# Performance work log

Hardware: AMD Instinct MI355X
Metric: run time of the kernel (lower is better)

## Reference

```python
import jax, jax.numpy as jnp
import numpy as np
from jax import lax

CHUNK = 256  # query chunk size (manual tiling block)

def setup_inputs() -> dict:
    key = jax.random.key(0)
    kq, kk, kv = jax.random.split(key, 3)
    shape = (2, 16, 2048, 128)  # [B, H, S, D]
    q = jax.random.normal(kq, shape, dtype=jnp.float32)
    k = jax.random.normal(kk, shape, dtype=jnp.float32)
    v = jax.random.normal(kv, shape, dtype=jnp.float32)
    return {"q": q, "k": k, "v": v}

def reference(q, k, v):
    # Chunked (memory-efficient) exact attention: softmax(QK^T/sqrt(D)) V,
    # computed one query block at a time so the full [S,S] score matrix
    # is never materialized.
    B, H, S, D = q.shape
    scale = jnp.asarray(1.0 / np.sqrt(D), dtype=q.dtype)
    n_chunks = S // CHUNK
    # [n_chunks, B, H, CHUNK, D]
    q_blocks = q.reshape(B, H, n_chunks, CHUNK, D).transpose(2, 0, 1, 3, 4)

    def step(carry, q_blk):
        # scores for this query block vs all keys: [B, H, CHUNK, S]
        s = jnp.einsum('bhqd,bhkd->bhqk', q_blk, k) * scale
        p = jax.nn.softmax(s, axis=-1)
        o = jnp.einsum('bhqk,bhkd->bhqd', p, v)
        return carry, o

    _, out_blocks = lax.scan(step, None, q_blocks)
    # [n_chunks, B, H, CHUNK, D] -> [B, H, S, D]
    out = out_blocks.transpose(1, 2, 0, 3, 4).reshape(B, H, S, D)
    return out
```

## Files before the change

### kernel.cpp

```cpp
#include <hip/hip_runtime.h>
#include <hip/hip_bf16.h>


typedef short short8 __attribute__((ext_vector_type(8)));
typedef float f32x16 __attribute__((ext_vector_type(16)));

#define MFMA32(a, b, c) __builtin_amdgcn_mfma_f32_32x32x16_bf16((a), (b), (c), 0, 0, 0)

#if __has_builtin(__builtin_amdgcn_exp2f)
#define EXP2(x) __builtin_amdgcn_exp2f(x)
#else
#define EXP2(x) exp2f(x)
#endif

constexpr int Dh  = 128;
constexpr int S_  = 2048;
constexpr int KVB = 64;
constexpr int NT  = S_ / KVB;
constexpr int WAVES = 8;
constexpr int QBLK  = 256;

__device__ __forceinline__ short f2bf(float f) {
    union { float f; unsigned u; } x; x.f = f;
    unsigned r = x.u + 0x7fffu + ((x.u >> 16) & 1u);
    return (short)(r >> 16);
}

__device__ __forceinline__ unsigned pkbf(float lo, float hi) {
    unsigned r;
    asm("v_cvt_pk_bf16_f32 %0, %1, %2" : "=v"(r) : "v"(lo), "v"(hi));
    return r;
}

__device__ __forceinline__ void pswap(unsigned &a, unsigned &b) {
    asm("v_permlane32_swap_b32 %0, %1" : "+v"(a), "+v"(b));
}

__device__ __forceinline__ void gload16(const void* g, void* l) {
    __builtin_amdgcn_global_load_lds(
        (const __attribute__((address_space(1))) unsigned int*)g,
        (__attribute__((address_space(3))) unsigned int*)l, 16, 0, 0);
}

__global__ __launch_bounds__(256) void prep_k(const float* __restrict__ K,
                                              short* __restrict__ Kz) {
    int idx = blockIdx.x * 256 + threadIdx.x;
    int b   = idx & 15;
    int s   = (idx >> 4) & (S_ - 1);
    int sb  = b ^ (s & 15);
    const float* src = K + (size_t)(idx >> 4) * Dh + sb * 8;
    float4 f0 = ((const float4*)src)[0];
    float4 f1 = ((const float4*)src)[1];
    short8 o;
    o[0] = f2bf(f0.x); o[1] = f2bf(f0.y); o[2] = f2bf(f0.z); o[3] = f2bf(f0.w);
    o[4] = f2bf(f1.x); o[5] = f2bf(f1.y); o[6] = f2bf(f1.z); o[7] = f2bf(f1.w);
    *(short8*)(Kz + (size_t)idx * 8) = o;
}

__global__ __launch_bounds__(256) void prep_v(const float* __restrict__ V,
                                              short* __restrict__ Vt) {
    __shared__ short tr[64][72];
    int bid = blockIdx.x;
    int dg = bid & 1, seg = (bid >> 1) & 31, bh = bid >> 6;
    int t = threadIdx.x;
    int s = t >> 2, d0 = (t & 3) * 16;
    const float* src = V + (size_t)(bh * S_ + seg * 64 + s) * Dh + dg * 64 + d0;
    #pragma unroll
    for (int i = 0; i < 16; i += 4) {
        float4 f = *(const float4*)(src + i);
        tr[d0 + i + 0][s] = f2bf(f.x); tr[d0 + i + 1][s] = f2bf(f.y);
        tr[d0 + i + 2][s] = f2bf(f.z); tr[d0 + i + 3][s] = f2bf(f.w);
    }
    __syncthreads();
    int d = t >> 2, j0 = (t & 3) * 2;
    size_t ob = ((size_t)(bh * 32 + seg) * 128 + dg * 64 + d) * 64;
    #pragma unroll
    for (int jj = 0; jj < 2; ++jj) {
        int j = j0 + jj;
        int sj = (j ^ (d & 7)) * 8;
        short8 val = *(const short8*)&tr[d][sj];
        *(short8*)(Vt + ob + j * 8) = val;
    }
}

__global__ __launch_bounds__(512, 2)
void mea_fwd6(const float* __restrict__ Qg, const short* __restrict__ Kz,
              const short* __restrict__ Vt, float* __restrict__ Og, int nqt) {
    __shared__ __align__(16) short kbuf[3][KVB * Dh];
    __shared__ __align__(16) short vbuf[3][Dh * KVB];
    __shared__ float bc_lds[WAVES][32];

    const int bid = blockIdx.x;
    const int cpx = (int)gridDim.x >> 3;
    const int swz = (bid & 7) * cpx + (bid >> 3);
    const int qt  = swz % nqt;
    const int bh  = swz / nqt;

    const int tid  = threadIdx.x;
    const int w    = tid >> 6;
    const int lane = tid & 63;
    const int l31  = lane & 31;
    const int hi   = lane >> 5;

    const size_t base = (size_t)bh * S_ * Dh;
    const int    qrow = qt * QBLK + w * 32 + l31;
    const float  QSC  = 0.08838834764831845f * 1.4426950408889634f;

    short8 qf[8];
    {
        const float* qp = Qg + base + (size_t)qrow * Dh;
        #pragma unroll
        for (int kc = 0; kc < 8; ++kc) {
            const float4 f0 = *(const float4*)(qp + kc * 16 + hi * 8);
            const float4 f1 = *(const float4*)(qp + kc * 16 + hi * 8 + 4);
            short8 a;
            a[0] = f2bf(f0.x * QSC); a[1] = f2bf(f0.y * QSC);
            a[2] = f2bf(f0.z * QSC); a[3] = f2bf(f0.w * QSC);
            a[4] = f2bf(f1.x * QSC); a[5] = f2bf(f1.y * QSC);
            a[6] = f2bf(f1.z * QSC); a[7] = f2bf(f1.w * QSC);
            qf[kc] = a;
        }
    }

    f32x16 oacc[4];
    #pragma unroll
    for (int dt = 0; dt < 4; ++dt)
        #pragma unroll
        for (int r = 0; r < 16; ++r) oacc[dt][r] = 0.f;
    float mrun = -1e30f, lpart = 0.f;

    const short* kt0 = Kz + base;
    const short* vt0 = Vt + base;

    short *kA = kbuf[0], *kB = kbuf[1], *kC = kbuf[2];
    short *vA = vbuf[0], *vB = vbuf[1], *vC = vbuf[2];

    auto STAGE = [&](short* kl, short* vl, int t) {
        const short* ks = kt0 + (size_t)t * (KVB * Dh);
        const short* vs = vt0 + (size_t)t * (Dh * KVB);
        #pragma unroll
        for (int i = 0; i < 2; ++i) {
            const int ou = (i * 8 + w) * 512;
            gload16(ks + ou + lane * 8, kl + ou);
            gload16(vs + ou + lane * 8, vl + ou);
        }
    };

    auto QKSTEP = [&](const short* kl, f32x16& A, f32x16& B) {
        #pragma unroll
        for (int r = 0; r < 16; ++r) { A[r] = 0.f; B[r] = 0.f; }
        __builtin_amdgcn_s_setprio(1);
        #pragma unroll
        for (int kc = 0; kc < 8; ++kc) {
            const int go = (((kc * 2 + hi) ^ (l31 & 15)) * 8);
            const short8 a0 = *(const short8*)&kl[l31 * Dh + go];
            const short8 a1 = *(const short8*)&kl[(32 + l31) * Dh + go];
            A = MFMA32(a0, qf[kc], A);
            B = MFMA32(a1, qf[kc], B);
        }
        __builtin_amdgcn_s_setprio(0);
    };

    auto SMPACK = [&](f32x16& sa, f32x16& sb, short8* pf) {
        float mxl = sa[0];
        #pragma unroll
        for (int r = 1; r < 16; ++r) mxl = fmaxf(mxl, sa[r]);
        #pragma unroll
        for (int r = 0; r < 16; ++r) mxl = fmaxf(mxl, sb[r]);
        if (__any(mxl > mrun + 8.0f)) {
            float mo   = fmaxf(mxl, __shfl_xor(mxl, 32));
            float mnew = fmaxf(mrun, mo);
            float rc   = EXP2(mrun - mnew);
            mrun = mnew;
            lpart *= rc;
            if (!hi) bc_lds[w][l31] = rc;
            #pragma unroll
            for (int m = 0; m < 4; ++m) {
                const float4 rcv = *(const float4*)&bc_lds[w][m * 8 + 4 * hi];
                #pragma unroll
                for (int t2 = 0; t2 < 4; ++t2) {
                    const float f = (&rcv.x)[t2];
                    #pragma unroll
                    for (int dt = 0; dt < 4; ++dt) oacc[dt][m * 4 + t2] *= f;
                }
            }
        }
        f32x16 pa, pb;
        float s0 = 0.f, s1 = 0.f;
        #pragma unroll
        for (int r = 0; r < 16; ++r) { pa[r] = EXP2(sa[r] - mrun); s0 += pa[r]; }
        #pragma unroll
        for (int r = 0; r < 16; ++r) { pb[r] = EXP2(sb[r] - mrun); s1 += pb[r]; }
        lpart += s0 + s1;
        #pragma unroll
        for (int kk = 0; kk < 2; ++kk) {
            unsigned a0 = pkbf(pa[kk * 8 + 0], pa[kk * 8 + 1]);
            unsigned a1 = pkbf(pa[kk * 8 + 2], pa[kk * 8 + 3]);
            unsigned b0 = pkbf(pa[kk * 8 + 4], pa[kk * 8 + 5]);
            unsigned b1 = pkbf(pa[kk * 8 + 6], pa[kk * 8 + 7]);
            pswap(a0, b0); pswap(a1, b1);
            unsigned wd[4] = {a0, a1, b0, b1};
            pf[kk] = *(const short8*)wd;
        }
        #pragma unroll
        for (int kk = 0; kk < 2; ++kk) {
            unsigned a0 = pkbf(pb[kk * 8 + 0], pb[kk * 8 + 1]);
            unsigned a1 = pkbf(pb[kk * 8 + 2], pb[kk * 8 + 3]);
            unsigned b0 = pkbf(pb[kk * 8 + 4], pb[kk * 8 + 5]);
            unsigned b1 = pkbf(pb[kk * 8 + 6], pb[kk * 8 + 7]);
            pswap(a0, b0); pswap(a1, b1);
            unsigned wd[4] = {a0, a1, b0, b1};
            pf[2 + kk] = *(const short8*)wd;
        }
    };

    auto PVSTEP = [&](const short* vl, const short8* pf) {
        __builtin_amdgcn_s_setprio(1);
        #pragma unroll
        for (int dt = 0; dt < 4; ++dt) {
            #pragma unroll
            for (int ks = 0; ks < 4; ++ks) {
                const short8 bv = *(const short8*)
                    &vl[(dt * 32 + l31) * KVB + (((ks * 2 + hi) ^ (l31 & 7)) * 8)];
                oacc[dt] = MFMA32(pf[ks], bv, oacc[dt]);
            }
        }
        __builtin_amdgcn_s_setprio(0);
    };

    auto BODY = [&](int t, f32x16& cA, f32x16& cB, f32x16& nA, f32x16& nB) {
        if (t + 2 < NT) STAGE(kC, vC, t + 2);
        QKSTEP(kB, nA, nB);
        short8 pf[4];
        SMPACK(cA, cB, pf);
        PVSTEP(vA, pf);
        __syncthreads();
        short* tk = kA; kA = kB; kB = kC; kC = tk;
        short* tv = vA; vA = vB; vB = vC; vC = tv;
    };

    STAGE(kA, vA, 0);
    STAGE(kB, vB, 1);
    __syncthreads();
    f32x16 s0A, s0B, s1A, s1B;
    QKSTEP(kA, s0A, s0B);

    #pragma unroll 1
    for (int kk = 0; kk < 15; ++kk) {
        BODY(2 * kk,     s0A, s0B, s1A, s1B);
        BODY(2 * kk + 1, s1A, s1B, s0A, s0B);
    }
    BODY(30, s0A, s0B, s1A, s1B);
    {
        short8 pf[4];
        SMPACK(s1A, s1B, pf);
        PVSTEP(vA, pf);
    }

    {
        const float tot = lpart + __shfl_xor(lpart, 32);
        if (!hi) bc_lds[w][l31] = 1.0f / tot;
    }
    float* op = Og + base;
    #pragma unroll
    for (int m = 0; m < 4; ++m) {
        const float4 li = *(const float4*)&bc_lds[w][m * 8 + 4 * hi];
        #pragma unroll
        for (int t2 = 0; t2 < 4; ++t2) {
            const int row  = m * 8 + 4 * hi + t2;
            const float lf = (&li.x)[t2];
            #pragma unroll
            for (int dt = 0; dt < 4; ++dt)
                op[(size_t)(qt * QBLK + w * 32 + row) * Dh + dt * 32 + l31]
                    = oacc[dt][m * 4 + t2] * lf;
        }
    }
}

typedef float f32x4 __attribute__((ext_vector_type(4)));
#define MFMA16(a, b, c) __builtin_amdgcn_mfma_f32_16x16x32_bf16((a), (b), (c), 0, 0, 0)
constexpr int FKVB = 32;
constexpr int FKP  = 136;
constexpr int FVP  = 40;
constexpr int FPP  = 40;

__global__ __launch_bounds__(256, 2)
void mea_fwd_fb(const float* __restrict__ Qg, const float* __restrict__ Kg,
                const float* __restrict__ Vg, float* __restrict__ Og,
                int S, int nqt) {
    __shared__ __align__(16) short k_lds[FKVB][FKP];
    __shared__ __align__(16) short vT_lds[Dh][FVP];
    __shared__ __align__(16) short p_lds[4][16][FPP];

    const int qt = blockIdx.x % nqt;
    const int bh = blockIdx.x / nqt;
    const int tid = threadIdx.x;
    const int w = tid >> 6, lane = tid & 63;
    const int lr = lane & 15, lg = lane >> 4;
    const size_t base = (size_t)bh * S * Dh;
    const int qrow0 = qt * 64 + w * 16;
    const float scale = 0.08838834764831845f;

    short8 qf[4];
    {
        const float* qp = Qg + base + (size_t)(qrow0 + lr) * Dh;
        #pragma unroll
        for (int kc = 0; kc < 4; ++kc) {
            const float4 f0 = *(const float4*)(qp + kc * 32 + lg * 8);
            const float4 f1 = *(const float4*)(qp + kc * 32 + lg * 8 + 4);
            short8 a;
            a[0] = f2bf(f0.x); a[1] = f2bf(f0.y); a[2] = f2bf(f0.z); a[3] = f2bf(f0.w);
            a[4] = f2bf(f1.x); a[5] = f2bf(f1.y); a[6] = f2bf(f1.z); a[7] = f2bf(f1.w);
            qf[kc] = a;
        }
    }
    f32x4 oacc[8];
    #pragma unroll
    for (int dt = 0; dt < 8; ++dt) oacc[dt] = (f32x4){0.f, 0.f, 0.f, 0.f};
    float mrun[4] = {-1e30f, -1e30f, -1e30f, -1e30f};
    float lrun[4] = {0.f, 0.f, 0.f, 0.f};
    const int sr = tid >> 3, sc = (tid & 7) * 16;

    for (int kv0 = 0; kv0 < S; kv0 += FKVB) {
        {
            const float* kp = Kg + base + (size_t)(kv0 + sr) * Dh + sc;
            const float* vp = Vg + base + (size_t)(kv0 + sr) * Dh + sc;
            short8 pk0, pk1;
            float4 f0 = ((const float4*)kp)[0], f1 = ((const float4*)kp)[1];
            float4 f2 = ((const float4*)kp)[2], f3 = ((const float4*)kp)[3];
            pk0[0] = f2bf(f0.x); pk0[1] = f2bf(f0.y); pk0[2] = f2bf(f0.z); pk0[3] = f2bf(f0.w);
            pk0[4] = f2bf(f1.x); pk0[5] = f2bf(f1.y); pk0[6] = f2bf(f1.z); pk0[7] = f2bf(f1.w);
            pk1[0] = f2bf(f2.x); pk1[1] = f2bf(f2.y); pk1[2] = f2bf(f2.z); pk1[3] = f2bf(f2.w);
            pk1[4] = f2bf(f3.x); pk1[5] = f2bf(f3.y); pk1[6] = f2bf(f3.z); pk1[7] = f2bf(f3.w);
            *(short8*)&k_lds[sr][sc] = pk0;
            *(short8*)&k_lds[sr][sc + 8] = pk1;
            #pragma unroll
            for (int i = 0; i < 4; ++i) {
                float4 f = ((const float4*)vp)[i];
                vT_lds[sc + 4 * i + 0][sr] = f2bf(f.x);
                vT_lds[sc + 4 * i + 1][sr] = f2bf(f.y);
                vT_lds[sc + 4 * i + 2][sr] = f2bf(f.z);
                vT_lds[sc + 4 * i + 3][sr] = f2bf(f.w);
            }
        }
        __syncthreads();
        f32x4 s0 = (f32x4){0.f,0.f,0.f,0.f}, s1 = (f32x4){0.f,0.f,0.f,0.f};
        #pragma unroll
        for (int kc = 0; kc < 4; ++kc) {
            short8 b0 = *(const short8*)&k_lds[lr][kc * 32 + lg * 8];
            short8 b1 = *(const short8*)&k_lds[16 + lr][kc * 32 + lg * 8];
            s0 = MFMA16(qf[kc], b0, s0);
            s1 = MFMA16(qf[kc], b1, s1);
        }
        float resc[4];
        #pragma unroll
        for (int r = 0; r < 4; ++r) {
            float mxv = fmaxf(s0[r], s1[r]);
            #pragma unroll
            for (int m = 1; m < 16; m <<= 1) mxv = fmaxf(mxv, __shfl_xor(mxv, m));
            float mnew = fmaxf(mrun[r], mxv * scale);
            float rc = __expf(mrun[r] - mnew);
            mrun[r] = mnew;
            float p0 = __expf(s0[r] * scale - mnew);
            float p1 = __expf(s1[r] * scale - mnew);
            float rs = p0 + p1;
            #pragma unroll
            for (int m = 1; m < 16; m <<= 1) rs += __shfl_xor(rs, m);
            lrun[r] = lrun[r] * rc + rs;
            resc[r] = rc;
            p_lds[w][lg * 4 + r][lr] = f2bf(p0);
            p_lds[w][lg * 4 + r][16 + lr] = f2bf(p1);
        }
        #pragma unroll
        for (int dt = 0; dt < 8; ++dt) {
            f32x4 o = oacc[dt];
            o[0] *= resc[0]; o[1] *= resc[1]; o[2] *= resc[2]; o[3] *= resc[3];
            oacc[dt] = o;
        }
        short8 ap = *(const short8*)&p_lds[w][lr][lg * 8];
        #pragma unroll
        for (int dt = 0; dt < 8; ++dt) {
            short8 bv = *(const short8*)&vT_lds[dt * 16 + lr][lg * 8];
            oacc[dt] = MFMA16(ap, bv, oacc[dt]);
        }
        __syncthreads();
    }
    float inv[4];
    #pragma unroll
    for (int r = 0; r < 4; ++r) inv[r] = 1.0f / lrun[r];
    float* op = Og + base;
    #pragma unroll
    for (int dt = 0; dt < 8; ++dt)
        #pragma unroll
        for (int r = 0; r < 4; ++r)
            op[(size_t)(qrow0 + lg * 4 + r) * Dh + dt * 16 + lr] = oacc[dt][r] * inv[r];
}

extern "C" void kernel_launch(void* const* d_in, const int* in_sizes, int n_in,
                              void* d_out, int out_size, void* d_ws, size_t ws_size,
                              hipStream_t stream) {
    const float* q = (const float*)d_in[0];
    const float* k = (const float*)d_in[1];
    const float* v = (const float*)d_in[2];
    float* o = (float*)d_out;

    const int BH  = in_sizes[0] / (S_ * Dh);
    const int nqt = S_ / QBLK;

    const size_t kz_bytes = (size_t)BH * S_ * Dh * sizeof(short);
    const size_t need = 2 * kz_bytes;

    if (ws_size >= need) {
        short* Kz = (short*)d_ws;
        short* Vt = (short*)((char*)d_ws + kz_bytes);
        hipLaunchKernelGGL(prep_k, dim3(BH * S_ * 16 / 256), dim3(256), 0, stream, k, Kz);
        hipLaunchKernelGGL(prep_v, dim3(BH * (S_ / 64) * 2), dim3(256), 0, stream, v, Vt);
        hipLaunchKernelGGL(mea_fwd6, dim3(BH * nqt), dim3(512), 0, stream, q, Kz, Vt, o, nqt);
    } else {
        hipLaunchKernelGGL(mea_fwd_fb, dim3(BH * (S_ / 64)), dim3(256), 0, stream,
                           q, k, v, o, S_, S_ / 64);
    }
}
```

Baseline: 95.49 us.

## Interleave softmax exp with PV MFMAs and fuse K/V prep kernels

The main loop now computes QK scores and immediately turns them into packed bf16 probabilities for the next step, while the PV MFMAs for the previous tile are split per output slice and interleaved with exp2 work. The aim is to overlap transcendental VALU work with matrix instructions. When a max rescale is needed, all PV MFMAs run first, then the rescale, then the exp. Separately, the K and V bf16 prep kernels are merged into one launch with a hardcoded block split at 4096, which removes one launch but assumes the K block count matches BH=32.

```diff
diff --git a/kernel.cpp b/kernel.cpp
--- a/kernel.cpp
+++ b/kernel.cpp
@@ -42,49 +42,50 @@
         (__attribute__((address_space(3))) unsigned int*)l, 16, 0, 0);
 }
 
-__global__ __launch_bounds__(256) void prep_k(const float* __restrict__ K,
-                                              short* __restrict__ Kz) {
-    int idx = blockIdx.x * 256 + threadIdx.x;
-    int b   = idx & 15;
-    int s   = (idx >> 4) & (S_ - 1);
-    int sb  = b ^ (s & 15);
-    const float* src = K + (size_t)(idx >> 4) * Dh + sb * 8;
-    float4 f0 = ((const float4*)src)[0];
-    float4 f1 = ((const float4*)src)[1];
-    short8 o;
-    o[0] = f2bf(f0.x); o[1] = f2bf(f0.y); o[2] = f2bf(f0.z); o[3] = f2bf(f0.w);
-    o[4] = f2bf(f1.x); o[5] = f2bf(f1.y); o[6] = f2bf(f1.z); o[7] = f2bf(f1.w);
-    *(short8*)(Kz + (size_t)idx * 8) = o;
-}
-
-__global__ __launch_bounds__(256) void prep_v(const float* __restrict__ V,
-                                              short* __restrict__ Vt) {
+__global__ __launch_bounds__(256) void prep_kv(const float* __restrict__ K,
+                                               const float* __restrict__ V,
+                                               short* __restrict__ Kz,
+                                               short* __restrict__ Vt) {
     __shared__ short tr[64][72];
-    int bid = blockIdx.x;
-    int dg = bid & 1, seg = (bid >> 1) & 31, bh = bid >> 6;
-    int t = threadIdx.x;
-    int s = t >> 2, d0 = (t & 3) * 16;
-    const float* src = V + (size_t)(bh * S_ + seg * 64 + s) * Dh + dg * 64 + d0;
-    #pragma unroll
-    for (int i = 0; i < 16; i += 4) {
-        float4 f = *(const float4*)(src + i);
-        tr[d0 + i + 0][s] = f2bf(f.x); tr[d0 + i + 1][s] = f2bf(f.y);
-        tr[d0 + i + 2][s] = f2bf(f.z); tr[d0 + i + 3][s] = f2bf(f.w);
-    }
-    __syncthreads();
-    int d = t >> 2, j0 = (t & 3) * 2;
-    size_t ob = ((size_t)(bh * 32 + seg) * 128 + dg * 64 + d) * 64;
-    #pragma unroll
-    for (int jj = 0; jj < 2; ++jj) {
-        int j = j0 + jj;
-        int sj = (j ^ (d & 7)) * 8;
-        short8 val = *(const short8*)&tr[d][sj];
-        *(short8*)(Vt + ob + j * 8) = val;
+    if (blockIdx.x < 4096) {
+        int idx = blockIdx.x * 256 + threadIdx.x;
+        int b   = idx & 15;
+        int s   = (idx >> 4) & (S_ - 1);
+        int sb  = b ^ (s & 15);
+        const float* src = K + (size_t)(idx >> 4) * Dh + sb * 8;
+        float4 f0 = ((const float4*)src)[0];
+        float4 f1 = ((const float4*)src)[1];
+        short8 o;
+        o[0] = f2bf(f0.x); o[1] = f2bf(f0.y); o[2] = f2bf(f0.z); o[3] = f2bf(f0.w);
+        o[4] = f2bf(f1.x); o[5] = f2bf(f1.y); o[6] = f2bf(f1.z); o[7] = f2bf(f1.w);
+        *(short8*)(Kz + (size_t)idx * 8) = o;
+    } else {
+        int bid = blockIdx.x - 4096;
+        int dg = bid & 1, seg = (bid >> 1) & 31, bh = bid >> 6;
+        int t = threadIdx.x;
+        int s = t >> 2, d0 = (t & 3) * 16;
+        const float* src = V + (size_t)(bh * S_ + seg * 64 + s) * Dh + dg * 64 + d0;
+        #pragma unroll
+        for (int i = 0; i < 16; i += 4) {
+            float4 f = *(const float4*)(src + i);
+            tr[d0 + i + 0][s] = f2bf(f.x); tr[d0 + i + 1][s] = f2bf(f.y);
+            tr[d0 + i + 2][s] = f2bf(f.z); tr[d0 + i + 3][s] = f2bf(f.w);
+        }
+        __syncthreads();
+        int d = t >> 2, j0 = (t & 3) * 2;
+        size_t ob = ((size_t)(bh * 32 + seg) * 128 + dg * 64 + d) * 64;
+        #pragma unroll
+        for (int jj = 0; jj < 2; ++jj) {
+            int j = j0 + jj;
+            int sj = (j ^ (d & 7)) * 8;
+            short8 val = *(const short8*)&tr[d][sj];
+            *(short8*)(Vt + ob + j * 8) = val;
+        }
     }
 }
 
 __global__ __launch_bounds__(512, 2)
-void mea_fwd6(const float* __restrict__ Qg, const short* __restrict__ Kz,
+void mea_fwd7(const float* __restrict__ Qg, const short* __restrict__ Kz,
               const short* __restrict__ Vt, float* __restrict__ Og, int nqt) {
     __shared__ __align__(16) short kbuf[3][KVB * Dh];
     __shared__ __align__(16) short vbuf[3][Dh * KVB];
@@ -161,79 +162,81 @@
         __builtin_amdgcn_s_setprio(0);
     };
 
-    auto SMPACK = [&](f32x16& sa, f32x16& sb, short8* pf) {
-        float mxl = sa[0];
-        #pragma unroll
-        for (int r = 1; r < 16; ++r) mxl = fmaxf(mxl, sa[r]);
-        #pragma unroll
-        for (int r = 0; r < 16; ++r) mxl = fmaxf(mxl, sb[r]);
-        if (__any(mxl > mrun + 8.0f)) {
-            float mo   = fmaxf(mxl, __shfl_xor(mxl, 32));
-            float mnew = fmaxf(mrun, mo);
-            float rc   = EXP2(mrun - mnew);
-            mrun = mnew;
-            lpart *= rc;
-            if (!hi) bc_lds[w][l31] = rc;
-            #pragma unroll
-            for (int m = 0; m < 4; ++m) {
-                const float4 rcv = *(const float4*)&bc_lds[w][m * 8 + 4 * hi];
-                #pragma unroll
-                for (int t2 = 0; t2 < 4; ++t2) {
-                    const float f = (&rcv.x)[t2];
-                    #pragma unroll
-                    for (int dt = 0; dt < 4; ++dt) oacc[dt][m * 4 + t2] *= f;
-                }
-            }
-        }
-        f32x16 pa, pb;
-        float s0 = 0.f, s1 = 0.f;
-        #pragma unroll
-        for (int r = 0; r < 16; ++r) { pa[r] = EXP2(sa[r] - mrun); s0 += pa[r]; }
-        #pragma unroll
-        for (int r = 0; r < 16; ++r) { pb[r] = EXP2(sb[r] - mrun); s1 += pb[r]; }
-        lpart += s0 + s1;
+    auto PVQ = [&](const short* vl, const short8* pf, f32x16& od, int dt) {
+        __builtin_amdgcn_s_setprio(1);
+        #pragma unroll
+        for (int ks = 0; ks < 4; ++ks) {
+            const short8 bv = *(const short8*)
+                &vl[(dt * 32 + l31) * KVB + (((ks * 2 + hi) ^ (l31 & 7)) * 8)];
+            od = MFMA32(pf[ks], bv, od);
+        }
+        __builtin_amdgcn_s_setprio(0);
+    };
+
+    auto EXPH = [&](f32x16& S, int h, float& sum) {
+        #pragma unroll
+        for (int r = 0; r < 8; ++r) {
+            const float p = EXP2(S[h * 8 + r] - mrun);
+            S[h * 8 + r] = p;
+            sum += p;
+        }
+    };
+
+    auto PACKH = [&](const f32x16& S, short8* pf2) {
         #pragma unroll
         for (int kk = 0; kk < 2; ++kk) {
-            unsigned a0 = pkbf(pa[kk * 8 + 0], pa[kk * 8 + 1]);
-            unsigned a1 = pkbf(pa[kk * 8 + 2], pa[kk * 8 + 3]);
-            unsigned b0 = pkbf(pa[kk * 8 + 4], pa[kk * 8 + 5]);
-            unsigned b1 = pkbf(pa[kk * 8 + 6], pa[kk * 8 + 7]);
+            unsigned a0 = pkbf(S[kk * 8 + 0], S[kk * 8 + 1]);
+            unsigned a1 = pkbf(S[kk * 8 + 2], S[kk * 8 + 3]);
+            unsigned b0 = pkbf(S[kk * 8 + 4], S[kk * 8 + 5]);
+            unsigned b1 = pkbf(S[kk * 8 + 6], S[kk * 8 + 7]);
             pswap(a0, b0); pswap(a1, b1);
             unsigned wd[4] = {a0, a1, b0, b1};
-            pf[kk] = *(const short8*)wd;
-        }
-        #pragma unroll
-        for (int kk = 0; kk < 2; ++kk) {
-            unsigned a0 = pkbf(pb[kk * 8 + 0], pb[kk * 8 + 1]);
-            unsigned a1 = pkbf(pb[kk * 8 + 2], pb[kk * 8 + 3]);
-            unsigned b0 = pkbf(pb[kk * 8 + 4], pb[kk * 8 + 5]);
-            unsigned b1 = pkbf(pb[kk * 8 + 6], pb[kk * 8 + 7]);
-            pswap(a0, b0); pswap(a1, b1);
-            unsigned wd[4] = {a0, a1, b0, b1};
-            pf[2 + kk] = *(const short8*)wd;
-        }
-    };
-
-    auto PVSTEP = [&](const short* vl, const short8* pf) {
-        __builtin_amdgcn_s_setprio(1);
-        #pragma unroll
-        for (int dt = 0; dt < 4; ++dt) {
+            pf2[kk] = *(const short8*)wd;
+        }
+    };
+
+    auto RESCALE = [&](float mxl) {
+        float mo   = fmaxf(mxl, __shfl_xor(mxl, 32));
+        float mnew = fmaxf(mrun, mo);
+        float rc   = EXP2(mrun - mnew);
+        mrun = mnew;
+        lpart *= rc;
+        if (!hi) bc_lds[w][l31] = rc;
+        #pragma unroll
+        for (int m = 0; m < 4; ++m) {
+            const float4 rcv = *(const float4*)&bc_lds[w][m * 8 + 4 * hi];
             #pragma unroll
-            for (int ks = 0; ks < 4; ++ks) {
-                const short8 bv = *(const short8*)
-                    &vl[(dt * 32 + l31) * KVB + (((ks * 2 + hi) ^ (l31 & 7)) * 8)];
-                oacc[dt] = MFMA32(pf[ks], bv, oacc[dt]);
+            for (int t2 = 0; t2 < 4; ++t2) {
+                const float f = (&rcv.x)[t2];
+                #pragma unroll
+                for (int dt = 0; dt < 4; ++dt) oacc[dt][m * 4 + t2] *= f;
             }
         }
-        __builtin_amdgcn_s_setprio(0);
-    };
-
-    auto BODY = [&](int t, f32x16& cA, f32x16& cB, f32x16& nA, f32x16& nB) {
+    };
+
+    auto BODY = [&](int t, const short8* pfC, short8* pfN) {
         if (t + 2 < NT) STAGE(kC, vC, t + 2);
-        QKSTEP(kB, nA, nB);
-        short8 pf[4];
-        SMPACK(cA, cB, pf);
-        PVSTEP(vA, pf);
+        f32x16 SA, SB;
+        QKSTEP(kB, SA, SB);
+        float mxl = SA[0];
+        #pragma unroll
+        for (int r = 1; r < 16; ++r) mxl = fmaxf(mxl, SA[r]);
+        #pragma unroll
+        for (int r = 0; r < 16; ++r) mxl = fmaxf(mxl, SB[r]);
+        float sum = 0.f;
+        if (!__any(mxl > mrun + 8.0f)) {
+            PVQ(vA, pfC, oacc[0], 0); EXPH(SA, 0, sum);
+            PVQ(vA, pfC, oacc[1], 1); EXPH(SA, 1, sum); PACKH(SA, pfN);
+            PVQ(vA, pfC, oacc[2], 2); EXPH(SB, 0, sum);
+            PVQ(vA, pfC, oacc[3], 3); EXPH(SB, 1, sum); PACKH(SB, pfN + 2);
+        } else {
+            PVQ(vA, pfC, oacc[0], 0); PVQ(vA, pfC, oacc[1], 1);
+            PVQ(vA, pfC, oacc[2], 2); PVQ(vA, pfC, oacc[3], 3);
+            RESCALE(mxl);
+            EXPH(SA, 0, sum); EXPH(SA, 1, sum); PACKH(SA, pfN);
+            EXPH(SB, 0, sum); EXPH(SB, 1, sum); PACKH(SB, pfN + 2);
+        }
+        lpart += sum;
         __syncthreads();
         short* tk = kA; kA = kB; kB = kC; kC = tk;
         short* tv = vA; vA = vB; vB = vC; vC = tv;
@@ -242,20 +245,30 @@
     STAGE(kA, vA, 0);
     STAGE(kB, vB, 1);
     __syncthreads();
-    f32x16 s0A, s0B, s1A, s1B;
-    QKSTEP(kA, s0A, s0B);
+    short8 pfA[4], pfB[4];
+    {
+        f32x16 SA, SB;
+        QKSTEP(kA, SA, SB);
+        float mxl = SA[0];
+        #pragma unroll
+        for (int r = 1; r < 16; ++r) mxl = fmaxf(mxl, SA[r]);
+        #pragma unroll
+        for (int r = 0; r < 16; ++r) mxl = fmaxf(mxl, SB[r]);
+        RESCALE(mxl);
+        float sum = 0.f;
+        EXPH(SA, 0, sum); EXPH(SA, 1, sum); PACKH(SA, pfA);
+        EXPH(SB, 0, sum); EXPH(SB, 1, sum); PACKH(SB, pfA + 2);
+        lpart += sum;
+    }
 
     #pragma unroll 1
     for (int kk = 0; kk < 15; ++kk) {
-        BODY(2 * kk,     s0A, s0B, s1A, s1B);
-        BODY(2 * kk + 1, s1A, s1B, s0A, s0B);
-    }
-    BODY(30, s0A, s0B, s1A, s1B);
-    {
-        short8 pf[4];
-        SMPACK(s1A, s1B, pf);
-        PVSTEP(vA, pf);
-    }
+        BODY(2 * kk,     pfA, pfB);
+        BODY(2 * kk + 1, pfB, pfA);
+    }
+    BODY(30, pfA, pfB);
+    PVQ(vA, pfB, oacc[0], 0); PVQ(vA, pfB, oacc[1], 1);
+    PVQ(vA, pfB, oacc[2], 2); PVQ(vA, pfB, oacc[3], 3);
 
     {
         const float tot = lpart + __shfl_xor(lpart, 32);
@@ -413,9 +426,10 @@
     if (ws_size >= need) {
         short* Kz = (short*)d_ws;
         short* Vt = (short*)((char*)d_ws + kz_bytes);
-        hipLaunchKernelGGL(prep_k, dim3(BH * S_ * 16 / 256), dim3(256), 0, stream, k, Kz);
-        hipLaunchKernelGGL(prep_v, dim3(BH * (S_ / 64) * 2), dim3(256), 0, stream, v, Vt);
-        hipLaunchKernelGGL(mea_fwd6, dim3(BH * nqt), dim3(512), 0, stream, q, Kz, Vt, o, nqt);
+        hipLaunchKernelGGL(prep_kv, dim3(4096 + BH * (S_ / 64) * 2), dim3(256),
+                           0, stream, k, v, Kz, Vt);
+        hipLaunchKernelGGL(mea_fwd7, dim3(BH * nqt), dim3(512), 0, stream,
+                           q, Kz, Vt, o, nqt);
     } else {
         hipLaunchKernelGGL(mea_fwd_fb, dim3(BH * (S_ / 64)), dim3(256), 0, stream,
                            q, k, v, o, S_, S_ / 64);
```

Result: slower. 135.6 us (+42.0%).
